# Kernel tuning notes

Measured on AMD Instinct MI355X. Metric: run time of the kernel, lower is better.

The kernel has to match this reference:

```python
import jax, jax.numpy as jnp
import numpy as np

B, N = 2, 4096
BN_EPS = 1e-5
INV_STD = np.float32(1.0 / np.sqrt(1.0 + BN_EPS))  # BN inference: running_mean=0, running_var=1


def pconv(x, w):
    # 1x1 Conv1d == per-point matmul: x [B,C,N], w [Cout,Cin] -> [B,Cout,N]
    return jnp.einsum('oc,bcn->bon', w, x)


def bn(x, g, b):
    # inference BatchNorm1d with mean=0, var=1
    return x * (INV_STD * g)[None, :, None] + b[None, :, None]


def sa_layer(x, qk_w, v_w, v_b, t_w, t_b, g, b):
    # PCT offset-attention. q_conv and k_conv share weights, so energy is a Gram matrix.
    xq = pconv(x, qk_w)                                   # [B, C//2, N]
    energy = jnp.einsum('bcn,bcm->bnm', xq, xq)           # [B, N, N]
    att = jax.nn.softmax(energy, axis=-1)
    att = att / (1e-9 + att.sum(axis=1, keepdims=True))   # extra L1 renorm over dim=1
    xv = pconv(x, v_w) + v_b[None, :, None]               # [B, C, N]
    x_r = jnp.einsum('bcn,bnm->bcm', xv, att)             # [B, C, N]
    # offset=True branch
    x_r = jax.nn.relu(bn(pconv(x - x_r, t_w) + t_b[None, :, None], g, b))
    return x + x_r


def _forward(x, conv1_w, bn1_g, bn1_b, conv2_w, bn2_g, bn2_b, conv3_w, bn3_g, bn3_b,
             pt1_w, pt1_g, pt1_b, pt2_w, pt2_g, pt2_b,
             sa1_qk, sa1_vw, sa1_vb, sa1_tw, sa1_tb, sa1_g, sa1_b,
             sa2_qk, sa2_vw, sa2_vb, sa2_tw, sa2_tb, sa2_g, sa2_b,
             cf_w, cf_g, cf_b, s1_w, s1_g, s1_b, s2_w, s2_g, s2_b, s3_w):
    h = jnp.transpose(x, (0, 2, 1))                       # [B, 3, N]
    h = jax.nn.relu(bn(pconv(h, conv1_w), bn1_g, bn1_b))  # [B, 64, N]
    h = jax.nn.relu(bn(pconv(h, conv2_w), bn2_g, bn2_b))  # [B, 128, N]
    h = jax.nn.relu(bn(pconv(h, conv3_w), bn3_g, bn3_b))  # [B, 256, N]
    # Point_Transformer_Last
    h = jax.nn.relu(bn(pconv(h, pt1_w), pt1_g, pt1_b))
    h = jax.nn.relu(bn(pconv(h, pt2_w), pt2_g, pt2_b))
    x1 = sa_layer(h, sa1_qk, sa1_vw, sa1_vb, sa1_tw, sa1_tb, sa1_g, sa1_b)
    x2 = sa_layer(x1, sa2_qk, sa2_vw, sa2_vb, sa2_tw, sa2_tb, sa2_g, sa2_b)
    # original forward reuses sa2's weights for layers 3 and 4
    x3 = sa_layer(x2, sa2_qk, sa2_vw, sa2_vb, sa2_tw, sa2_tb, sa2_g, sa2_b)
    x4 = sa_layer(x3, sa2_qk, sa2_vw, sa2_vb, sa2_tw, sa2_tb, sa2_g, sa2_b)
    h = jnp.concatenate([x1, x2, x3, x4], axis=1)         # [B, 1024, N]
    face = jax.nn.leaky_relu(bn(pconv(h, cf_w), cf_g, cf_b), 0.2)  # [B, 512, N]
    gmax = jnp.max(face, axis=2, keepdims=True)           # adaptive_max_pool1d(.,1)
    h = jnp.concatenate([face, jnp.broadcast_to(gmax, face.shape)], axis=1)  # [B, 1024, N]
    h = jax.nn.leaky_relu(bn(pconv(h, s1_w), s1_g, s1_b), 0.2)
    h = jax.nn.leaky_relu(bn(pconv(h, s2_w), s2_g, s2_b), 0.2)
    h = pconv(h, s3_w)                                    # [B, 50, N]
    return jnp.transpose(h, (0, 2, 1))                    # [B, N, 50]


def setup_inputs() -> dict:
    key = jax.random.key(0)
    kit = iter(jax.random.split(key, 80))
    def W(co, ci):
        return jax.random.normal(next(kit), (co, ci), dtype=jnp.float32) / np.float32(np.sqrt(ci))
    def G(c):
        return 1.0 + 0.1 * jax.random.normal(next(kit), (c,), dtype=jnp.float32)
    def Bv(c):
        return 0.1 * jax.random.normal(next(kit), (c,), dtype=jnp.float32)
    d = {}
    d['x'] = jax.random.normal(next(kit), (B, N, 3), dtype=jnp.float32)
    d['conv1_w'] = W(64, 3);   d['bn1_g'] = G(64);  d['bn1_b'] = Bv(64)
    d['conv2_w'] = W(128, 64); d['bn2_g'] = G(128); d['bn2_b'] = Bv(128)
    d['conv3_w'] = W(256, 128); d['bn3_g'] = G(256); d['bn3_b'] = Bv(256)
    d['pt1_w'] = W(256, 256); d['pt1_g'] = G(256); d['pt1_b'] = Bv(256)
    d['pt2_w'] = W(256, 256); d['pt2_g'] = G(256); d['pt2_b'] = Bv(256)
    for p in ('sa1', 'sa2'):
        d[p + '_qk'] = 0.1 * W(128, 256)  # small scale keeps softmax unsaturated
        d[p + '_vw'] = W(256, 256); d[p + '_vb'] = Bv(256)
        d[p + '_tw'] = W(256, 256); d[p + '_tb'] = Bv(256)
        d[p + '_g'] = G(256); d[p + '_b'] = Bv(256)
    d['cf_w'] = W(512, 1024); d['cf_g'] = G(512); d['cf_b'] = Bv(512)
    d['s1_w'] = W(512, 1024); d['s1_g'] = G(512); d['s1_b'] = Bv(512)
    d['s2_w'] = W(256, 512); d['s2_g'] = G(256); d['s2_b'] = Bv(256)
    d['s3_w'] = W(50, 256)
    return d


def reference(x, conv1_w, bn1_g, bn1_b, conv2_w, bn2_g, bn2_b, conv3_w, bn3_g, bn3_b,
              pt1_w, pt1_g, pt1_b, pt2_w, pt2_g, pt2_b,
              sa1_qk, sa1_vw, sa1_vb, sa1_tw, sa1_tb, sa1_g, sa1_b,
              sa2_qk, sa2_vw, sa2_vb, sa2_tw, sa2_tb, sa2_g, sa2_b,
              cf_w, cf_g, cf_b, s1_w, s1_g, s1_b, s2_w, s2_g, s2_b, s3_w):
    return _forward(x, conv1_w, bn1_g, bn1_b, conv2_w, bn2_g, bn2_b, conv3_w, bn3_g, bn3_b,
                    pt1_w, pt1_g, pt1_b, pt2_w, pt2_g, pt2_b,
                    sa1_qk, sa1_vw, sa1_vb, sa1_tw, sa1_tb, sa1_g, sa1_b,
                    sa2_qk, sa2_vw, sa2_vb, sa2_tw, sa2_tb, sa2_g, sa2_b,
                    cf_w, cf_g, cf_b, s1_w, s1_g, s1_b, s2_w, s2_g, s2_b, s3_w)
```

## Files before the change

kernel.cpp:

```cpp
#include <hip/hip_runtime.h>
#include <hip/hip_bf16.h>


#define NPTS 4096
#define BATCH 2
#define MSPLIT 4
#define RSSPLIT 8
static constexpr float INV_STD = 0.9999950000374997f;

__device__ __forceinline__ float bf2f(unsigned short u) {
    return __uint_as_float(((unsigned int)u) << 16);
}
__device__ __forceinline__ unsigned short f2bf(float f) {
    unsigned int x = __float_as_uint(f);
    unsigned int r = (x + 0x7FFFu + ((x >> 16) & 1u)) >> 16;
    return (unsigned short)r;
}

typedef __attribute__((ext_vector_type(8))) short short8;
typedef __attribute__((ext_vector_type(4))) float f32x4;

struct WSplit {
    const float* src[14];
    int n[14];
    long long off[14];
};

__global__ __launch_bounds__(256)
void presplit_k(WSplit d, unsigned short* __restrict__ wbuf)
{
    int wi = blockIdx.y;
    int i = blockIdx.x * 256 + threadIdx.x;
    int n = d.n[wi];
    if (i >= n) return;
    float v = d.src[wi][i];
    unsigned short h = f2bf(v);
    unsigned short* dst = wbuf + d.off[wi];
    dst[i] = h;
    dst[n + i] = f2bf(v - bf2f(h));
}

__global__ __launch_bounds__(256)
void gemm_nt_split(const unsigned short* __restrict__ A, long long a_bs, int a_lda, long long a_po,
                   const unsigned short* __restrict__ B, long long b_bs, int b_lda, long long b_po,
                   void* __restrict__ Cp, long long c_bs, int c_ld, long long c_po,
                   int Nb, int K,
                   const float* __restrict__ bias, int bias_mode,
                   const float* __restrict__ bng, const float* __restrict__ bnb,
                   const unsigned short* __restrict__ res, long long res_bs, int res_ld, long long res_po,
                   int act, int out_mode)
{
    __shared__ unsigned short As[2][64 * 64];
    __shared__ unsigned short Bs[2][64 * 64];
    const int b = blockIdx.z;
    const int m0 = blockIdx.y * 64, n0 = blockIdx.x * 64;
    const int t = threadIdx.x;
    const int lane = t & 63, w = t >> 6;
    const int wr = (w >> 1) * 32, wc = (w & 1) * 32;
    const int ml = lane & 15, q = lane >> 4;

    f32x4 acc[2][2] = {};

    for (int k0 = 0; k0 < K; k0 += 64) {
        __syncthreads();
        #pragma unroll
        for (int e = 0; e < 2; e++) {
            int idx = t + e * 256;
            int row = idx >> 3, blk = idx & 7;
            int gblk = blk ^ (row & 7);
            {
                const unsigned short* s = A + (long long)b * a_bs
                                        + (long long)(m0 + row) * a_lda + k0 + gblk * 8;
                *(int4*)(&As[0][row * 64 + blk * 8]) = *(const int4*)s;
                *(int4*)(&As[1][row * 64 + blk * 8]) = *(const int4*)(s + a_po);
            }
            {
                int4 hi = make_int4(0, 0, 0, 0), lo = make_int4(0, 0, 0, 0);
                if ((n0 + row) < Nb) {
                    const unsigned short* s = B + (long long)b * b_bs
                                            + (long long)(n0 + row) * b_lda + k0 + gblk * 8;
                    hi = *(const int4*)s; lo = *(const int4*)(s + b_po);
                }
                *(int4*)(&Bs[0][row * 64 + blk * 8]) = hi;
                *(int4*)(&Bs[1][row * 64 + blk * 8]) = lo;
            }
        }
        __syncthreads();
        #pragma unroll
        for (int kk = 0; kk < 2; kk++) {
            short8 ah[2], al[2], bh[2], bl[2];
            #pragma unroll
            for (int it = 0; it < 2; it++) {
                int row = wr + it * 16 + ml;
                int slot = (kk * 4 + q) ^ (row & 7);
                ah[it] = *(const short8*)(&As[0][row * 64 + slot * 8]);
                al[it] = *(const short8*)(&As[1][row * 64 + slot * 8]);
            }
            #pragma unroll
            for (int jt = 0; jt < 2; jt++) {
                int row = wc + jt * 16 + ml;
                int slot = (kk * 4 + q) ^ (row & 7);
                bh[jt] = *(const short8*)(&Bs[0][row * 64 + slot * 8]);
                bl[jt] = *(const short8*)(&Bs[1][row * 64 + slot * 8]);
            }
            #pragma unroll
            for (int it = 0; it < 2; it++)
                #pragma unroll
                for (int jt = 0; jt < 2; jt++) {
                    acc[it][jt] = __builtin_amdgcn_mfma_f32_16x16x32_bf16(ah[it], bh[jt], acc[it][jt], 0, 0, 0);
                    acc[it][jt] = __builtin_amdgcn_mfma_f32_16x16x32_bf16(ah[it], bl[jt], acc[it][jt], 0, 0, 0);
                    acc[it][jt] = __builtin_amdgcn_mfma_f32_16x16x32_bf16(al[it], bh[jt], acc[it][jt], 0, 0, 0);
                }
        }
    }

    #pragma unroll
    for (int it = 0; it < 2; it++)
        #pragma unroll
        for (int jt = 0; jt < 2; jt++)
            #pragma unroll
            for (int r = 0; r < 4; r++) {
                int rg = m0 + wr + it * 16 + q * 4 + r;
                int cg = n0 + wc + jt * 16 + ml;
                float y = acc[it][jt][r];
                if (bias) {
                    if (bias_mode == 3)      y += bias[rg];
                    else if (bias_mode == 2) y += bias[b * Nb + cg];
                    else                     y += bias[cg];
                }
                if (bng) y = y * (INV_STD * bng[cg]) + bnb[cg];
                if (act == 1) y = fmaxf(y, 0.f);
                else if (act == 2) y = (y > 0.f) ? y : 0.2f * y;
                if (res) {
                    long long ri_ = (long long)b * res_bs + (long long)rg * res_ld + cg;
                    y += bf2f(res[ri_]) + bf2f(res[res_po + ri_]);
                }
                long long ci = (long long)b * c_bs + (long long)rg * c_ld + cg;
                if (out_mode == 0) {
                    unsigned short* C = (unsigned short*)Cp;
                    unsigned short h = f2bf(y);
                    C[ci] = h;
                    C[c_po + ci] = f2bf(y - bf2f(h));
                } else if (out_mode == 1) {
                    ((unsigned short*)Cp)[ci] = f2bf(y);
                } else {
                    if (cg < Nb) ((float*)Cp)[ci] = y;
                }
            }
}

__global__ __launch_bounds__(256)
void rs_k(const unsigned short* __restrict__ xq, float* __restrict__ rs)
{
    __shared__ unsigned short Kq[2][64 * 64];
    const int b = blockIdx.z;
    const int p0 = blockIdx.y * 64;
    const int m_beg = blockIdx.x * (NPTS / RSSPLIT);
    const unsigned short* xqB = xq + (long long)b * NPTS * 128;
    const int t = threadIdx.x;
    const int lane = t & 63, w = t >> 6;
    const int pw = w * 16;
    const int ml = lane & 15, q = lane >> 4;

    short8 af[4];
    #pragma unroll
    for (int ks = 0; ks < 4; ks++)
        af[ks] = *(const short8*)(xqB + (long long)(p0 + pw + ml) * 128 + ks * 32 + q * 8);

    float rsum[4] = {0.f, 0.f, 0.f, 0.f};

    for (int m0 = m_beg; m0 < m_beg + NPTS / RSSPLIT; m0 += 64) {
        __syncthreads();
        #pragma unroll
        for (int e = 0; e < 4; e++) {
            int idx = t + e * 256;
            int sub = idx >> 9, row = (idx >> 3) & 63, blk = idx & 7;
            int gblk = blk ^ (row & 7);
            *(int4*)(&Kq[sub][row * 64 + blk * 8]) =
                *(const int4*)(xqB + (long long)(m0 + row) * 128 + sub * 64 + gblk * 8);
        }
        __syncthreads();
        f32x4 acc[4] = {};
        #pragma unroll
        for (int ks = 0; ks < 4; ks++) {
            int kh = ks >> 1, kk = ks & 1;
            #pragma unroll
            for (int jt = 0; jt < 4; jt++) {
                int row = jt * 16 + ml;
                int slot = (kk * 4 + q) ^ (row & 7);
                short8 bf = *(const short8*)(&Kq[kh][row * 64 + slot * 8]);
                acc[jt] = __builtin_amdgcn_mfma_f32_16x16x32_bf16(af[ks], bf, acc[jt], 0, 0, 0);
            }
        }
        #pragma unroll
        for (int jt = 0; jt < 4; jt++)
            #pragma unroll
            for (int r = 0; r < 4; r++)
                rsum[r] += __expf(acc[jt][r]);
    }
    #pragma unroll
    for (int r = 0; r < 4; r++) {
        float s = rsum[r];
        s += __shfl_xor(s, 1); s += __shfl_xor(s, 2);
        s += __shfl_xor(s, 4); s += __shfl_xor(s, 8);
        if (ml == 0) atomicAdd(&rs[b * NPTS + p0 + pw + q * 4 + r], s);
    }
}

__global__ __launch_bounds__(256)
void attn_pv(const unsigned short* __restrict__ xq,
             const unsigned short* __restrict__ xv,
             const float* __restrict__ rinv,
             float* __restrict__ part,
             float* __restrict__ cs)
{
    __shared__ unsigned short Kq[2][64 * 64];
    __shared__ unsigned short Vv[256 * 64];
    __shared__ unsigned short Pl[64][72];
    const int z = blockIdx.z, b = z / MSPLIT, ms = z % MSPLIT;
    const int p0 = blockIdx.y * 64;
    const unsigned short* xqB = xq + (long long)b * NPTS * 128;
    const unsigned short* xvB = xv + (long long)b * 256 * NPTS;
    const float* riB = rinv + b * NPTS;
    const int t = threadIdx.x;
    const int lane = t & 63, w = t >> 6;
    const int pw = w * 16;
    const int cw = w * 64;
    const int ml = lane & 15, q = lane >> 4;

    short8 af[4];
    #pragma unroll
    for (int ks = 0; ks < 4; ks++)
        af[ks] = *(const short8*)(xqB + (long long)(p0 + pw + ml) * 128 + ks * 32 + q * 8);

    f32x4 pv[4][4] = {};
    float csr[4] = {0.f, 0.f, 0.f, 0.f};

    const int m_beg = ms * (NPTS / MSPLIT);
    for (int m0 = m_beg; m0 < m_beg + NPTS / MSPLIT; m0 += 64) {
        __syncthreads();
        #pragma unroll
        for (int e = 0; e < 4; e++) {
            int idx = t + e * 256;
            int sub = idx >> 9, row = (idx >> 3) & 63, blk = idx & 7;
            int gblk = blk ^ (row & 7);
            *(int4*)(&Kq[sub][row * 64 + blk * 8]) =
                *(const int4*)(xqB + (long long)(m0 + row) * 128 + sub * 64 + gblk * 8);
        }
        #pragma unroll
        for (int e = 0; e < 8; e++) {
            int idx = t + e * 256;
            int row = idx >> 3, blk = idx & 7;
            int gblk = blk ^ (row & 7);
            *(int4*)(&Vv[row * 64 + blk * 8]) =
                *(const int4*)(xvB + (long long)row * NPTS + m0 + gblk * 8);
        }
        __syncthreads();
        f32x4 acc[4] = {};
        #pragma unroll
        for (int ks = 0; ks < 4; ks++) {
            int kh = ks >> 1, kk = ks & 1;
            #pragma unroll
            for (int jt = 0; jt < 4; jt++) {
                int row = jt * 16 + ml;
                int slot = (kk * 4 + q) ^ (row & 7);
                short8 bf = *(const short8*)(&Kq[kh][row * 64 + slot * 8]);
                acc[jt] = __builtin_amdgcn_mfma_f32_16x16x32_bf16(af[ks], bf, acc[jt], 0, 0, 0);
            }
        }
        #pragma unroll
        for (int jt = 0; jt < 4; jt++) {
            float rv = riB[m0 + jt * 16 + ml];
            #pragma unroll
            for (int r = 0; r < 4; r++) {
                float pvv = __expf(acc[jt][r]) * rv;
                csr[r] += pvv;
                Pl[pw + q * 4 + r][jt * 16 + ml] = f2bf(pvv);
            }
        }
        __syncthreads();
        #pragma unroll
        for (int kk = 0; kk < 2; kk++) {
            short8 ap[4];
            #pragma unroll
            for (int pst = 0; pst < 4; pst++)
                ap[pst] = *(const short8*)(&Pl[pst * 16 + ml][kk * 32 + q * 8]);
            #pragma unroll
            for (int jt = 0; jt < 4; jt++) {
                int row = cw + jt * 16 + ml;
                int slot = (kk * 4 + q) ^ (row & 7);
                short8 bv = *(const short8*)(&Vv[row * 64 + slot * 8]);
                #pragma unroll
                for (int pst = 0; pst < 4; pst++)
                    pv[pst][jt] = __builtin_amdgcn_mfma_f32_16x16x32_bf16(
                        ap[pst], bv, pv[pst][jt], 0, 0, 0);
            }
        }
    }
    #pragma unroll
    for (int r = 0; r < 4; r++) {
        float s = csr[r];
        s += __shfl_xor(s, 1); s += __shfl_xor(s, 2);
        s += __shfl_xor(s, 4); s += __shfl_xor(s, 8);
        if (ml == 0) atomicAdd(&cs[b * NPTS + p0 + pw + q * 4 + r], s);
    }
    float* C = part + (long long)z * ((long long)NPTS * 256);
    #pragma unroll
    for (int pst = 0; pst < 4; pst++)
        #pragma unroll
        for (int jt = 0; jt < 4; jt++)
            #pragma unroll
            for (int r = 0; r < 4; r++) {
                int rg = p0 + pst * 16 + q * 4 + r;
                int cg = cw + jt * 16 + ml;
                C[(long long)rg * 256 + cg] = pv[pst][jt][r];
            }
}

__global__ __launch_bounds__(256)
void conv1_k(const float* __restrict__ x, const float* __restrict__ w,
             const float* __restrict__ g, const float* __restrict__ bb,
             unsigned short* __restrict__ h, long long h_po)
{
    int b = blockIdx.y;
    int p = blockIdx.x * 4 + (threadIdx.x >> 6);
    int c = threadIdx.x & 63;
    const float* xp = x + ((long long)b * NPTS + p) * 3;
    float y = xp[0] * w[c * 3] + xp[1] * w[c * 3 + 1] + xp[2] * w[c * 3 + 2];
    y = y * (INV_STD * g[c]) + bb[c];
    y = fmaxf(y, 0.f);
    long long i = ((long long)b * NPTS + p) * 64 + c;
    unsigned short hi = f2bf(y);
    h[i] = hi;
    h[h_po + i] = f2bf(y - bf2f(hi));
}

__global__ __launch_bounds__(256)
void zero_k(float* __restrict__ p, int n)
{
    int i = blockIdx.x * 256 + threadIdx.x;
    if (i < n) p[i] = 0.f;
}

__global__ __launch_bounds__(256)
void recip_k(const float* __restrict__ rs, float* __restrict__ ri, int n)
{
    int i = blockIdx.x * 256 + threadIdx.x;
    if (i < n) ri[i] = 1.f / rs[i];
}

__global__ __launch_bounds__(256)
void diff_k(const unsigned short* __restrict__ xin, long long x_bs, int x_ld, long long x_po,
            const float* __restrict__ part, const float* __restrict__ cs,
            unsigned short* __restrict__ d, long long d_po)
{
    long long i = (long long)blockIdx.x * 256 + threadIdx.x;
    int b = blockIdx.y;
    int p = (int)(i >> 8), c = (int)(i & 255);
    long long xi = (long long)b * x_bs + (long long)p * x_ld + c;
    float xv = bf2f(xin[xi]) + bf2f(xin[x_po + xi]);
    float xr = 0.f;
    #pragma unroll
    for (int ks = 0; ks < MSPLIT; ks++)
        xr += part[((long long)(b * MSPLIT + ks)) * ((long long)NPTS * 256) + i];
    float denom = 1e-9f + cs[b * NPTS + p];
    float v = xv - xr / denom;
    long long di = (long long)b * NPTS * 256 + i;
    unsigned short hi = f2bf(v);
    d[di] = hi;
    d[d_po + di] = f2bf(v - bf2f(hi));
}

__global__ __launch_bounds__(256)
void gmaxp_k(const unsigned short* __restrict__ face, long long f_po, float* __restrict__ pm)
{
    int c = blockIdx.x * 256 + threadIdx.x;
    int ch = blockIdx.y;
    int b = blockIdx.z;
    float m = -3.4e38f;
    for (int j = 0; j < 256; j++) {
        long long i = ((long long)b * NPTS + ch * 256 + j) * 512 + c;
        m = fmaxf(m, bf2f(face[i]) + bf2f(face[f_po + i]));
    }
    pm[((long long)b * 16 + ch) * 512 + c] = m;
}

__global__ __launch_bounds__(256)
void gmaxr_k(const float* __restrict__ pm, float* __restrict__ gm)
{
    int idx = blockIdx.x * 256 + threadIdx.x;
    int b = idx >> 9, c = idx & 511;
    float m = -3.4e38f;
    for (int ch = 0; ch < 16; ch++)
        m = fmaxf(m, pm[((long long)b * 16 + ch) * 512 + c]);
    gm[idx] = m;
}

__global__ __launch_bounds__(256)
void bias2_k(const float* __restrict__ w, const float* __restrict__ g, float* __restrict__ b2)
{
    int o = blockIdx.x * 256 + threadIdx.x;
    int b = blockIdx.y;
    if (o >= 512) return;
    float s = 0.f;
    for (int c = 0; c < 512; c++) s += w[(long long)o * 1024 + 512 + c] * g[b * 512 + c];
    b2[b * 512 + o] = s;
}

extern "C" void kernel_launch(void* const* d_in, const int* in_sizes, int n_in,
                              void* d_out, int out_size, void* d_ws, size_t ws_size,
                              hipStream_t stream)
{
    const float* x       = (const float*)d_in[0];
    const float* conv1_w = (const float*)d_in[1];
    const float* bn1_g   = (const float*)d_in[2];
    const float* bn1_b   = (const float*)d_in[3];
    const float* conv2_w = (const float*)d_in[4];
    const float* bn2_g   = (const float*)d_in[5];
    const float* bn2_b   = (const float*)d_in[6];
    const float* conv3_w = (const float*)d_in[7];
    const float* bn3_g   = (const float*)d_in[8];
    const float* bn3_b   = (const float*)d_in[9];
    const float* pt1_w   = (const float*)d_in[10];
    const float* pt1_g   = (const float*)d_in[11];
    const float* pt1_b   = (const float*)d_in[12];
    const float* pt2_w   = (const float*)d_in[13];
    const float* pt2_g   = (const float*)d_in[14];
    const float* pt2_b   = (const float*)d_in[15];
    const float* sa_qk[2] = {(const float*)d_in[16], (const float*)d_in[23]};
    const float* sa_vw[2] = {(const float*)d_in[17], (const float*)d_in[24]};
    const float* sa_vb[2] = {(const float*)d_in[18], (const float*)d_in[25]};
    const float* sa_tw[2] = {(const float*)d_in[19], (const float*)d_in[26]};
    const float* sa_tb[2] = {(const float*)d_in[20], (const float*)d_in[27]};
    const float* sa_g[2]  = {(const float*)d_in[21], (const float*)d_in[28]};
    const float* sa_b[2]  = {(const float*)d_in[22], (const float*)d_in[29]};
    const float* cf_w = (const float*)d_in[30];
    const float* cf_g = (const float*)d_in[31];
    const float* cf_b = (const float*)d_in[32];
    const float* s1_w = (const float*)d_in[33];
    const float* s1_g = (const float*)d_in[34];
    const float* s1_b = (const float*)d_in[35];
    const float* s2_w = (const float*)d_in[36];
    const float* s2_g = (const float*)d_in[37];
    const float* s2_b = (const float*)d_in[38];
    const float* s3_w = (const float*)d_in[39];

    char* base = (char*)d_ws;
    size_t off = 0;
    auto alloc = [&](size_t bytes) -> void* {
        void* p = base + off;
        off = (off + bytes + 255) & ~(size_t)255;
        return p;
    };
    const long long N = NPTS;
    const long long PO64   = (long long)BATCH * N * 64;
    const long long PO128  = (long long)BATCH * N * 128;
    const long long PO256  = (long long)BATCH * N * 256;
    const long long PO512  = (long long)BATCH * N * 512;
    const long long PO1024 = (long long)BATCH * N * 1024;

    unsigned short* S1  = (unsigned short*)alloc(2 * PO256 * 2);
    unsigned short* S2  = (unsigned short*)alloc(2 * PO256 * 2);
    unsigned short* Dv  = (unsigned short*)alloc(2 * PO256 * 2);
    unsigned short* cat = (unsigned short*)alloc(2 * PO1024 * 2);
    unsigned short* face = (unsigned short*)alloc(2 * PO512 * 2);
    unsigned short* xq  = (unsigned short*)alloc((size_t)BATCH * N * 128 * 2);
    unsigned short* xv  = (unsigned short*)alloc((size_t)BATCH * 256 * N * 2);
    unsigned short* s1b = (unsigned short*)alloc(2 * PO512 * 2);
    unsigned short* s2b = (unsigned short*)alloc(2 * PO256 * 2);
    float* part = (float*)alloc((size_t)BATCH * MSPLIT * N * 256 * 4);
    float* rs = (float*)alloc((size_t)BATCH * N * 4);
    float* cs = (float*)alloc((size_t)BATCH * N * 4);
    float* ri = (float*)alloc((size_t)BATCH * N * 4);
    float* pm = (float*)alloc((size_t)BATCH * 16 * 512 * 4);
    float* gm = (float*)alloc((size_t)BATCH * 512 * 4);
    float* b2 = (float*)alloc((size_t)BATCH * 512 * 4);
    unsigned short* wb = (unsigned short*)alloc((size_t)3400000 * 2);

    WSplit wd;
    const float* wsrc[14] = {conv2_w, conv3_w, pt1_w, pt2_w, sa_qk[0], sa_qk[1],
                             sa_vw[0], sa_vw[1], sa_tw[0], sa_tw[1], cf_w, s1_w, s2_w, s3_w};
    int wn[14] = {128*64, 256*128, 256*256, 256*256, 128*256, 128*256,
                  256*256, 256*256, 256*256, 256*256, 512*1024, 512*1024, 256*512, 50*256};
    long long wo[14]; long long acc_ = 0;
    for (int i = 0; i < 14; i++) { wd.src[i] = wsrc[i]; wd.n[i] = wn[i]; wd.off[i] = acc_; wo[i] = acc_; acc_ += 2LL * wn[i]; }
    presplit_k<<<dim3((512*1024 + 255) / 256, 14), 256, 0, stream>>>(wd, wb);
    auto W = [&](int i) { return wb + wo[i]; };

    auto nt = [&](const unsigned short* A, long long a_bs, int a_lda, long long a_po,
                  const unsigned short* B, long long b_bs, int b_lda, long long b_po,
                  void* C, long long c_bs, int c_ld, long long c_po,
                  int Mrows, int Nb, int K,
                  const float* bias, int bias_mode,
                  const float* bng, const float* bnb,
                  const unsigned short* res, long long res_bs, int res_ld, long long res_po,
                  int act, int out_mode) {
        dim3 g((Nb + 63) / 64, Mrows / 64, BATCH);
        gemm_nt_split<<<g, 256, 0, stream>>>(A, a_bs, a_lda, a_po, B, b_bs, b_lda, b_po,
                                             C, c_bs, c_ld, c_po, Nb, K,
                                             bias, bias_mode, bng, bnb,
                                             res, res_bs, res_ld, res_po, act, out_mode);
    };

    conv1_k<<<dim3(NPTS / 4, BATCH), 256, 0, stream>>>(x, conv1_w, bn1_g, bn1_b, S1, PO64);
    nt(S1, N * 64, 64, PO64,    W(0), 0, 64, wn[0],  S2, N * 128, 128, PO128,
       NPTS, 128, 64,  nullptr, 0, bn2_g, bn2_b, nullptr, 0, 0, 0, 1, 0);
    nt(S2, N * 128, 128, PO128, W(1), 0, 128, wn[1], S1, N * 256, 256, PO256,
       NPTS, 256, 128, nullptr, 0, bn3_g, bn3_b, nullptr, 0, 0, 0, 1, 0);
    nt(S1, N * 256, 256, PO256, W(2), 0, 256, wn[2], S2, N * 256, 256, PO256,
       NPTS, 256, 256, nullptr, 0, pt1_g, pt1_b, nullptr, 0, 0, 0, 1, 0);
    nt(S2, N * 256, 256, PO256, W(3), 0, 256, wn[3], S1, N * 256, 256, PO256,
       NPTS, 256, 256, nullptr, 0, pt2_g, pt2_b, nullptr, 0, 0, 0, 1, 0);

    for (int i = 0; i < 4; i++) {
        int p = (i == 0) ? 0 : 1;
        const unsigned short* xin = (i == 0) ? S1 : cat + (size_t)(i - 1) * 256;
        long long xin_bs = (i == 0) ? N * 256 : N * 1024;
        int xin_ld = (i == 0) ? 256 : 1024;
        long long xin_po = (i == 0) ? PO256 : PO1024;

        nt(xin, xin_bs, xin_ld, xin_po, W(4 + p), 0, 256, wn[4 + p],
           xq, N * 128, 128, 0, NPTS, 128, 256,
           nullptr, 0, nullptr, nullptr, nullptr, 0, 0, 0, 0, 1);
        nt(W(6 + p), 0, 256, wn[6 + p], xin, xin_bs, xin_ld, xin_po,
           xv, 256 * N, NPTS, 0, 256, NPTS, 256,
           sa_vb[p], 3, nullptr, nullptr, nullptr, 0, 0, 0, 0, 1);
        zero_k<<<(2 * BATCH * NPTS + 255) / 256, 256, 0, stream>>>(rs, 2 * BATCH * NPTS);
        rs_k<<<dim3(RSSPLIT, NPTS / 64, BATCH), 256, 0, stream>>>(xq, rs);
        recip_k<<<(BATCH * NPTS + 255) / 256, 256, 0, stream>>>(rs, ri, BATCH * NPTS);
        attn_pv<<<dim3(1, NPTS / 64, BATCH * MSPLIT), 256, 0, stream>>>(
            xq, xv, ri, part, cs);
        diff_k<<<dim3(NPTS * 256 / 256, BATCH), 256, 0, stream>>>(
            xin, xin_bs, xin_ld, xin_po, part, cs, Dv, PO256);
        nt(Dv, N * 256, 256, PO256, W(8 + p), 0, 256, wn[8 + p],
           cat + (size_t)i * 256, N * 1024, 1024, PO1024,
           NPTS, 256, 256, sa_tb[p], 1, sa_g[p], sa_b[p],
           xin, xin_bs, xin_ld, xin_po, 1, 0);
    }

    nt(cat, N * 1024, 1024, PO1024, W(10), 0, 1024, wn[10],
       face, N * 512, 512, PO512, NPTS, 512, 1024,
       nullptr, 0, cf_g, cf_b, nullptr, 0, 0, 0, 2, 0);
    gmaxp_k<<<dim3(2, 16, BATCH), 256, 0, stream>>>(face, PO512, pm);
    gmaxr_k<<<dim3(BATCH * 512 / 256), 256, 0, stream>>>(pm, gm);
    bias2_k<<<dim3(2, BATCH), 256, 0, stream>>>(s1_w, gm, b2);
    nt(face, N * 512, 512, PO512, W(11), 0, 1024, wn[11],
       s1b, N * 512, 512, PO512, NPTS, 512, 512,
       b2, 2, s1_g, s1_b, nullptr, 0, 0, 0, 2, 0);
    nt(s1b, N * 512, 512, PO512, W(12), 0, 512, wn[12],
       s2b, N * 256, 256, PO256, NPTS, 256, 512,
       nullptr, 0, s2_g, s2_b, nullptr, 0, 0, 0, 2, 0);
    nt(s2b, N * 256, 256, PO256, W(13), 0, 256, wn[13],
       d_out, N * 50, 50, 0, NPTS, 50, 256,
       nullptr, 0, nullptr, nullptr, nullptr, 0, 0, 0, 0, 2);
}
```

Before: 841.3 us.

## Use async global-to-LDS loads and split attention PV over channel halves

Replaces register-staged global-to-shared copies in the GEMM, row-sum and attention kernels with direct global_load_lds transfers. It also splits the attention PV kernel across two channel halves, doubling the grid and halving the per-block V tile and accumulators, with only one half accumulating column sums. This is meant to cut VGPR pressure and load latency and to raise occupancy. The cost is that each half recomputes the QK energy and exp, and the GEMM B load loses its Nb bounds guard, which could read out of range for ragged N.

```diff
diff --git a/kernel.cpp b/kernel.cpp
--- a/kernel.cpp
+++ b/kernel.cpp
@@ -15,6 +15,14 @@
     unsigned int x = __float_as_uint(f);
     unsigned int r = (x + 0x7FFFu + ((x >> 16) & 1u)) >> 16;
     return (unsigned short)r;
+}
+
+__device__ __forceinline__ void async16(const unsigned short* g, unsigned short* l)
+{
+    __builtin_amdgcn_global_load_lds(
+        (const __attribute__((address_space(1))) unsigned int*)(const void*)g,
+        (__attribute__((address_space(3))) unsigned int*)(void*)l,
+        16, 0, 0);
 }
 
 typedef __attribute__((ext_vector_type(8))) short short8;
@@ -68,22 +76,15 @@
             int idx = t + e * 256;
             int row = idx >> 3, blk = idx & 7;
             int gblk = blk ^ (row & 7);
-            {
-                const unsigned short* s = A + (long long)b * a_bs
-                                        + (long long)(m0 + row) * a_lda + k0 + gblk * 8;
-                *(int4*)(&As[0][row * 64 + blk * 8]) = *(const int4*)s;
-                *(int4*)(&As[1][row * 64 + blk * 8]) = *(const int4*)(s + a_po);
-            }
-            {
-                int4 hi = make_int4(0, 0, 0, 0), lo = make_int4(0, 0, 0, 0);
-                if ((n0 + row) < Nb) {
-                    const unsigned short* s = B + (long long)b * b_bs
-                                            + (long long)(n0 + row) * b_lda + k0 + gblk * 8;
-                    hi = *(const int4*)s; lo = *(const int4*)(s + b_po);
-                }
-                *(int4*)(&Bs[0][row * 64 + blk * 8]) = hi;
-                *(int4*)(&Bs[1][row * 64 + blk * 8]) = lo;
-            }
+            int lofs = (e * 256 + (t & 192)) * 8;
+            const unsigned short* sA = A + (long long)b * a_bs
+                                     + (long long)(m0 + row) * a_lda + k0 + gblk * 8;
+            const unsigned short* sB = B + (long long)b * b_bs
+                                     + (long long)(n0 + row) * b_lda + k0 + gblk * 8;
+            async16(sA,        &As[0][0] + lofs);
+            async16(sA + a_po, &As[1][0] + lofs);
+            async16(sB,        &Bs[0][0] + lofs);
+            async16(sB + b_po, &Bs[1][0] + lofs);
         }
         __syncthreads();
         #pragma unroll
@@ -176,8 +177,9 @@
             int idx = t + e * 256;
             int sub = idx >> 9, row = (idx >> 3) & 63, blk = idx & 7;
             int gblk = blk ^ (row & 7);
-            *(int4*)(&Kq[sub][row * 64 + blk * 8]) =
-                *(const int4*)(xqB + (long long)(m0 + row) * 128 + sub * 64 + gblk * 8);
+            int lofs = (e * 256 + (t & 192)) * 8;
+            async16(xqB + (long long)(m0 + row) * 128 + sub * 64 + gblk * 8,
+                    &Kq[0][0] + lofs);
         }
         __syncthreads();
         f32x4 acc[4] = {};
@@ -215,9 +217,10 @@
              float* __restrict__ cs)
 {
     __shared__ unsigned short Kq[2][64 * 64];
-    __shared__ unsigned short Vv[256 * 64];
+    __shared__ unsigned short Vv[128 * 64];
     __shared__ unsigned short Pl[64][72];
     const int z = blockIdx.z, b = z / MSPLIT, ms = z % MSPLIT;
+    const int c0 = blockIdx.x * 128;
     const int p0 = blockIdx.y * 64;
     const unsigned short* xqB = xq + (long long)b * NPTS * 128;
     const unsigned short* xvB = xv + (long long)b * 256 * NPTS;
@@ -225,15 +228,16 @@
     const int t = threadIdx.x;
     const int lane = t & 63, w = t >> 6;
     const int pw = w * 16;
-    const int cw = w * 64;
+    const int cw = w * 32;
     const int ml = lane & 15, q = lane >> 4;
+    const bool do_cs = (blockIdx.x == 0);
 
     short8 af[4];
     #pragma unroll
     for (int ks = 0; ks < 4; ks++)
         af[ks] = *(const short8*)(xqB + (long long)(p0 + pw + ml) * 128 + ks * 32 + q * 8);
 
-    f32x4 pv[4][4] = {};
+    f32x4 pv[4][2] = {};
     float csr[4] = {0.f, 0.f, 0.f, 0.f};
 
     const int m_beg = ms * (NPTS / MSPLIT);
@@ -244,16 +248,17 @@
             int idx = t + e * 256;
             int sub = idx >> 9, row = (idx >> 3) & 63, blk = idx & 7;
             int gblk = blk ^ (row & 7);
-            *(int4*)(&Kq[sub][row * 64 + blk * 8]) =
-                *(const int4*)(xqB + (long long)(m0 + row) * 128 + sub * 64 + gblk * 8);
-        }
-        #pragma unroll
-        for (int e = 0; e < 8; e++) {
+            int lofs = (e * 256 + (t & 192)) * 8;
+            async16(xqB + (long long)(m0 + row) * 128 + sub * 64 + gblk * 8,
+                    &Kq[0][0] + lofs);
+        }
+        #pragma unroll
+        for (int e = 0; e < 4; e++) {
             int idx = t + e * 256;
             int row = idx >> 3, blk = idx & 7;
             int gblk = blk ^ (row & 7);
-            *(int4*)(&Vv[row * 64 + blk * 8]) =
-                *(const int4*)(xvB + (long long)row * NPTS + m0 + gblk * 8);
+            int lofs = (e * 256 + (t & 192)) * 8;
+            async16(xvB + (long long)(c0 + row) * NPTS + m0 + gblk * 8, Vv + lofs);
         }
         __syncthreads();
         f32x4 acc[4] = {};
@@ -270,10 +275,10 @@
         }
         #pragma unroll
         for (int jt = 0; jt < 4; jt++) {
-            float rv = riB[m0 + jt * 16 + ml];
+            float rvm = riB[m0 + jt * 16 + ml];
             #pragma unroll
             for (int r = 0; r < 4; r++) {
-                float pvv = __expf(acc[jt][r]) * rv;
+                float pvv = __expf(acc[jt][r]) * rvm;
                 csr[r] += pvv;
                 Pl[pw + q * 4 + r][jt * 16 + ml] = f2bf(pvv);
             }
@@ -286,7 +291,7 @@
             for (int pst = 0; pst < 4; pst++)
                 ap[pst] = *(const short8*)(&Pl[pst * 16 + ml][kk * 32 + q * 8]);
             #pragma unroll
-            for (int jt = 0; jt < 4; jt++) {
+            for (int jt = 0; jt < 2; jt++) {
                 int row = cw + jt * 16 + ml;
                 int slot = (kk * 4 + q) ^ (row & 7);
                 short8 bv = *(const short8*)(&Vv[row * 64 + slot * 8]);
@@ -297,22 +302,24 @@
             }
         }
     }
-    #pragma unroll
-    for (int r = 0; r < 4; r++) {
-        float s = csr[r];
-        s += __shfl_xor(s, 1); s += __shfl_xor(s, 2);
-        s += __shfl_xor(s, 4); s += __shfl_xor(s, 8);
-        if (ml == 0) atomicAdd(&cs[b * NPTS + p0 + pw + q * 4 + r], s);
+    if (do_cs) {
+        #pragma unroll
+        for (int r = 0; r < 4; r++) {
+            float s = csr[r];
+            s += __shfl_xor(s, 1); s += __shfl_xor(s, 2);
+            s += __shfl_xor(s, 4); s += __shfl_xor(s, 8);
+            if (ml == 0) atomicAdd(&cs[b * NPTS + p0 + pw + q * 4 + r], s);
+        }
     }
     float* C = part + (long long)z * ((long long)NPTS * 256);
     #pragma unroll
     for (int pst = 0; pst < 4; pst++)
         #pragma unroll
-        for (int jt = 0; jt < 4; jt++)
+        for (int jt = 0; jt < 2; jt++)
             #pragma unroll
             for (int r = 0; r < 4; r++) {
                 int rg = p0 + pst * 16 + q * 4 + r;
-                int cg = cw + jt * 16 + ml;
+                int cg = c0 + cw + jt * 16 + ml;
                 C[(long long)rg * 256 + cg] = pv[pst][jt][r];
             }
 }
@@ -528,7 +535,7 @@
         zero_k<<<(2 * BATCH * NPTS + 255) / 256, 256, 0, stream>>>(rs, 2 * BATCH * NPTS);
         rs_k<<<dim3(RSSPLIT, NPTS / 64, BATCH), 256, 0, stream>>>(xq, rs);
         recip_k<<<(BATCH * NPTS + 255) / 256, 256, 0, stream>>>(rs, ri, BATCH * NPTS);
-        attn_pv<<<dim3(1, NPTS / 64, BATCH * MSPLIT), 256, 0, stream>>>(
+        attn_pv<<<dim3(2, NPTS / 64, BATCH * MSPLIT), 256, 0, stream>>>(
             xq, xv, ri, part, cs);
         diff_k<<<dim3(NPTS * 256 / 256, BATCH), 256, 0, stream>>>(
             xin, xin_bs, xin_ld, xin_po, part, cs, Dv, PO256);
```

Result: slower. 906.6 us (+7.8%).
